# Performance work log

Measured on AMD Instinct MI355X. Metric: run time of the kernel, lower is better.

Reference implementation:

```python
import jax, jax.numpy as jnp
import numpy as np

N = 8192
IN_F = 512
OUT_F = 256
POW = 2


def setup_inputs() -> dict:
    key = jax.random.key(0)
    k1, k2, k3, k4 = jax.random.split(key, 4)
    stdv = 1.0 / np.sqrt(OUT_F)
    inputs = {
        "input": jax.random.normal(k1, (N, IN_F), dtype=jnp.float32),
        "adj": jax.random.uniform(k2, (N, N), dtype=jnp.float32),
        "weight": jax.random.uniform(k3, (IN_F, OUT_F), dtype=jnp.float32, minval=-stdv, maxval=stdv),
        "bias": jax.random.uniform(k4, (OUT_F,), dtype=jnp.float32, minval=-stdv, maxval=stdv),
    }
    return inputs


def reference(input, adj, weight, bias):
    # K_adj = adj ** pow (elementwise power, as torch's ** on a dense tensor)
    k_adj = adj ** POW
    # support = X @ W  -> [N, out_features]
    support = jnp.einsum("ni,io->no", input, weight)
    # output = K_adj @ support -> [N, out_features]
    out = jnp.einsum("nm,mo->no", k_adj, support) + bias
    # F.elu with default alpha=1.0
    return jnp.where(out > 0, out, jnp.expm1(out))
```

## Files before the change

### kernel.cpp

```cpp
#include <hip/hip_runtime.h>
#include <cstdint>
#include <cstddef>

#define N_NODES 8192
#define INF 512
#define OUTF 256
#define SPLITK 8
#define MSLICE (N_NODES / SPLITK)

typedef _Float16 f16;
typedef _Float16 f16x8 __attribute__((ext_vector_type(8)));
typedef float f32x4 __attribute__((ext_vector_type(4)));

__device__ __forceinline__ void async_copy16(void* lds_dst, const void* g_src) {
  __builtin_amdgcn_global_load_lds(
      (const __attribute__((address_space(1))) void*)g_src,
      (__attribute__((address_space(3))) void*)lds_dst,
      16, 0, 0);
}

__device__ __forceinline__ float elu(float x) { return x > 0.f ? x : expm1f(x); }

__global__ __launch_bounds__(256) void cast_x(const float* __restrict__ X,
                                              f16* __restrict__ Xh) {
  const int idx = blockIdx.x * 256 + threadIdx.x;
  f32x4 v0 = ((const f32x4*)X)[idx * 2];
  f32x4 v1 = ((const f32x4*)X)[idx * 2 + 1];
  f16x8 h;
#pragma unroll
  for (int u = 0; u < 4; ++u) {
    h[u] = (f16)v0[u];
    h[4 + u] = (f16)v1[u];
  }
  ((f16x8*)Xh)[idx] = h;
}

__global__ __launch_bounds__(256) void transpose_w(const float* __restrict__ W,
                                                   f16* __restrict__ WhT) {
  const int idx = blockIdx.x * 256 + threadIdx.x;
  const int o = idx >> 9, i = idx & 511;
  WhT[idx] = (f16)W[i * OUTF + o];
}

__global__ __launch_bounds__(256) void gemm1(const f16* __restrict__ WhT,
                                             const f16* __restrict__ Xh,
                                             f16* __restrict__ supT) {
  __shared__ __align__(16) f16 Asm[64 * 64];
  __shared__ __align__(16) f16 Bsm[128 * 64];
  const int t = threadIdx.x;
  const int wave = t >> 6, lane = t & 63;
  const int q = lane >> 4, r = lane & 15;
  const int lrow = lane >> 3, lchunk = lane & 7;
  const int o0 = blockIdx.x * 64, m0 = blockIdx.y * 128;

  f32x4 acc[4][2];
#pragma unroll
  for (int i = 0; i < 4; ++i)
#pragma unroll
    for (int j = 0; j < 2; ++j) acc[i][j] = (f32x4){0.f, 0.f, 0.f, 0.f};

  for (int kt = 0; kt < 8; ++kt) {
    const int k0 = kt * 64;
#pragma unroll
    for (int op = 0; op < 2; ++op) {
      const int row = (wave * 2 + op) * 8 + lrow;
      const f16* src = WhT + (size_t)(o0 + row) * INF + k0 + (lchunk ^ lrow) * 8;
      async_copy16(Asm + (wave * 2 + op) * 8 * 64, src);
    }
#pragma unroll
    for (int op = 0; op < 4; ++op) {
      const int row = (wave * 4 + op) * 8 + lrow;
      const f16* src = Xh + (size_t)(m0 + row) * INF + k0 + (lchunk ^ lrow) * 8;
      async_copy16(Bsm + (wave * 4 + op) * 8 * 64, src);
    }
    __syncthreads();
#pragma unroll
    for (int s = 0; s < 2; ++s) {
      const int pc = ((s * 4 + q) ^ (r & 7)) * 8;
      f16x8 af[4], bf[2];
#pragma unroll
      for (int i = 0; i < 4; ++i) af[i] = *(const f16x8*)&Asm[(i * 16 + r) * 64 + pc];
#pragma unroll
      for (int j = 0; j < 2; ++j)
        bf[j] = *(const f16x8*)&Bsm[(wave * 32 + j * 16 + r) * 64 + pc];
#pragma unroll
      for (int i = 0; i < 4; ++i)
#pragma unroll
        for (int j = 0; j < 2; ++j)
          acc[i][j] = __builtin_amdgcn_mfma_f32_16x16x32_f16(af[i], bf[j],
                                                             acc[i][j], 0, 0, 0);
    }
    __syncthreads();
  }
#pragma unroll
  for (int i = 0; i < 4; ++i)
#pragma unroll
    for (int j = 0; j < 2; ++j) {
      const int m = m0 + wave * 32 + j * 16 + r;
#pragma unroll
      for (int g = 0; g < 4; ++g)
        supT[(size_t)(o0 + i * 16 + q * 4 + g) * N_NODES + m] = (f16)acc[i][j][g];
    }
}

template <bool ATOMIC>
__global__ __launch_bounds__(256, 4) void gemm2(const float* __restrict__ adj,
                                                const f16* __restrict__ supT,
                                                float* __restrict__ outp) {
  __shared__ __align__(16) f16 Asm[64 * 64];
  __shared__ __align__(16) f16 Bsm[256 * 64];
  const int t = threadIdx.x;
  const int wave = t >> 6, lane = t & 63;
  const int q = lane >> 4, r = lane & 15;
  const int n0 = blockIdx.x * 64;
  const size_t m_base = (size_t)blockIdx.y * MSLICE;

  f32x4 acc[4][4];
#pragma unroll
  for (int i = 0; i < 4; ++i)
#pragma unroll
    for (int j = 0; j < 4; ++j) acc[i][j] = (f32x4){0.f, 0.f, 0.f, 0.f};

  const int a_row = t >> 2;
  const int a_c0 = (t & 3) * 2;
  const float* aptr = adj + (size_t)(n0 + a_row) * N_NODES + m_base + (t & 3) * 16;
  const int b_o = wave * 64 + (lane >> 3);
  const int b_kb = lane & 7;

  for (int kt = 0; kt < MSLICE / 64; ++kt) {
#pragma unroll
    for (int j = 0; j < 8; ++j) {
      const int o = b_o + j * 8;
      const int kb = b_kb ^ (o & 7);
      const f16* src = supT + (size_t)o * N_NODES + m_base + kt * 64 + kb * 8;
      async_copy16(Bsm + (wave * 64 + j * 8) * 64, src);
    }
    {
      const float* ap = aptr + kt * 64;
      f32x4 v0 = *(const f32x4*)(ap + 0);
      f32x4 v1 = *(const f32x4*)(ap + 4);
      f32x4 v2 = *(const f32x4*)(ap + 8);
      f32x4 v3 = *(const f32x4*)(ap + 12);
      f16x8 h0, h1;
#pragma unroll
      for (int u = 0; u < 4; ++u) {
        h0[u] = (f16)(v0[u] * v0[u]);
        h0[4 + u] = (f16)(v1[u] * v1[u]);
        h1[u] = (f16)(v2[u] * v2[u]);
        h1[4 + u] = (f16)(v3[u] * v3[u]);
      }
      *(f16x8*)&Asm[a_row * 64 + ((a_c0 ^ (a_row & 7)) * 8)] = h0;
      *(f16x8*)&Asm[a_row * 64 + (((a_c0 + 1) ^ (a_row & 7)) * 8)] = h1;
    }
    __syncthreads();
#pragma unroll
    for (int s = 0; s < 2; ++s) {
      const int pc = ((s * 4 + q) ^ (r & 7)) * 8;
      f16x8 af[4], bf[4];
#pragma unroll
      for (int i = 0; i < 4; ++i) af[i] = *(const f16x8*)&Asm[(i * 16 + r) * 64 + pc];
#pragma unroll
      for (int j = 0; j < 4; ++j)
        bf[j] = *(const f16x8*)&Bsm[(wave * 64 + j * 16 + r) * 64 + pc];
#pragma unroll
      for (int i = 0; i < 4; ++i)
#pragma unroll
        for (int j = 0; j < 4; ++j)
          acc[i][j] = __builtin_amdgcn_mfma_f32_16x16x32_f16(af[i], bf[j],
                                                             acc[i][j], 0, 0, 0);
    }
    __syncthreads();
  }
  float* base = ATOMIC ? outp : outp + (size_t)blockIdx.y * N_NODES * OUTF;
#pragma unroll
  for (int i = 0; i < 4; ++i)
#pragma unroll
    for (int g = 0; g < 4; ++g) {
      const int n = n0 + i * 16 + q * 4 + g;
      float* orow = base + (size_t)n * OUTF + wave * 64 + r;
#pragma unroll
      for (int j = 0; j < 4; ++j) {
        if (ATOMIC)
          atomicAdd(orow + j * 16, acc[i][j][g]);
        else
          orow[j * 16] = acc[i][j][g];
      }
    }
}

__global__ __launch_bounds__(256) void reduce_elu(const float* __restrict__ P,
                                                  const float* __restrict__ bias,
                                                  float* __restrict__ out) {
  const int idx = blockIdx.x * 256 + threadIdx.x;
  f32x4 s = (f32x4){0.f, 0.f, 0.f, 0.f};
#pragma unroll
  for (int y = 0; y < SPLITK; ++y)
    s += ((const f32x4*)(P + (size_t)y * N_NODES * OUTF))[idx];
  const f32x4 b = ((const f32x4*)bias)[idx & 63];
  f32x4 v;
#pragma unroll
  for (int u = 0; u < 4; ++u) v[u] = elu(s[u] + b[u]);
  ((f32x4*)out)[idx] = v;
}

__global__ __launch_bounds__(256) void bias_elu(float* __restrict__ out,
                                                const float* __restrict__ bias) {
  const int idx = blockIdx.x * 256 + threadIdx.x;
  f32x4 v = ((const f32x4*)out)[idx];
  const f32x4 b = ((const f32x4*)bias)[idx & 63];
#pragma unroll
  for (int u = 0; u < 4; ++u) v[u] = elu(v[u] + b[u]);
  ((f32x4*)out)[idx] = v;
}

extern "C" void kernel_launch(void* const* d_in, const int* in_sizes, int n_in,
                              void* d_out, int out_size, void* d_ws, size_t ws_size,
                              hipStream_t stream) {
  const float* X = (const float*)d_in[0];
  const float* adj = (const float*)d_in[1];
  const float* W = (const float*)d_in[2];
  const float* bias = (const float*)d_in[3];
  float* out = (float*)d_out;

  char* ws = (char*)d_ws;
  f16* supT = (f16*)(ws + 0);
  f16* Xh = (f16*)(ws + (4u << 20));
  f16* WhT = (f16*)(ws + (12u << 20));
  float* P = (float*)(ws + (16u << 20));
  const size_t need = (80u << 20);

  cast_x<<<N_NODES * INF / 8 / 256, 256, 0, stream>>>(X, Xh);
  transpose_w<<<INF * OUTF / 256, 256, 0, stream>>>(W, WhT);
  gemm1<<<dim3(OUTF / 64, N_NODES / 128), 256, 0, stream>>>(WhT, Xh, supT);
  if (ws_size >= need) {
    gemm2<false><<<dim3(N_NODES / 64, SPLITK), 256, 0, stream>>>(adj, supT, P);
    reduce_elu<<<N_NODES * OUTF / 4 / 256, 256, 0, stream>>>(P, bias, out);
  } else {
    hipMemsetAsync(d_out, 0, (size_t)out_size * sizeof(float), stream);
    gemm2<true><<<dim3(N_NODES / 64, SPLITK), 256, 0, stream>>>(adj, supT, out);
    bias_elu<<<N_NODES * OUTF / 4 / 256, 256, 0, stream>>>(out, bias);
  }
}
```

Measured before the change: 443.4 us.

## Fuse X cast into gemm1 and store split-K partials in f16

Removes the separate cast_x kernel by loading fp32 X directly in gemm1 and converting it to f16 while staging into LDS, with gemm1 tiles reduced to 64x64. Split-K partial sums from gemm2 are now written as f16 and reduced in fp32, which halves partial-buffer traffic and shrinks the workspace requirement. The cost is lower precision in the partial sums and a smaller gemm1 tile with less data reuse.

```diff
diff --git a/kernel.cpp b/kernel.cpp
--- a/kernel.cpp
+++ b/kernel.cpp
@@ -10,6 +10,7 @@
 
 typedef _Float16 f16;
 typedef _Float16 f16x8 __attribute__((ext_vector_type(8)));
+typedef _Float16 f16x4 __attribute__((ext_vector_type(4)));
 typedef float f32x4 __attribute__((ext_vector_type(4)));
 
 __device__ __forceinline__ void async_copy16(void* lds_dst, const void* g_src) {
@@ -21,43 +22,31 @@
 
 __device__ __forceinline__ float elu(float x) { return x > 0.f ? x : expm1f(x); }
 
-__global__ __launch_bounds__(256) void cast_x(const float* __restrict__ X,
-                                              f16* __restrict__ Xh) {
-  const int idx = blockIdx.x * 256 + threadIdx.x;
-  f32x4 v0 = ((const f32x4*)X)[idx * 2];
-  f32x4 v1 = ((const f32x4*)X)[idx * 2 + 1];
-  f16x8 h;
-#pragma unroll
-  for (int u = 0; u < 4; ++u) {
-    h[u] = (f16)v0[u];
-    h[4 + u] = (f16)v1[u];
-  }
-  ((f16x8*)Xh)[idx] = h;
-}
-
-__global__ __launch_bounds__(256) void transpose_w(const float* __restrict__ W,
-                                                   f16* __restrict__ WhT) {
+__global__ __launch_bounds__(256) void prep_w(const float* __restrict__ W,
+                                              f16* __restrict__ WhT) {
   const int idx = blockIdx.x * 256 + threadIdx.x;
   const int o = idx >> 9, i = idx & 511;
   WhT[idx] = (f16)W[i * OUTF + o];
 }
 
 __global__ __launch_bounds__(256) void gemm1(const f16* __restrict__ WhT,
-                                             const f16* __restrict__ Xh,
+                                             const float* __restrict__ X,
                                              f16* __restrict__ supT) {
   __shared__ __align__(16) f16 Asm[64 * 64];
-  __shared__ __align__(16) f16 Bsm[128 * 64];
+  __shared__ __align__(16) f16 Bsm[64 * 64];
   const int t = threadIdx.x;
   const int wave = t >> 6, lane = t & 63;
   const int q = lane >> 4, r = lane & 15;
   const int lrow = lane >> 3, lchunk = lane & 7;
-  const int o0 = blockIdx.x * 64, m0 = blockIdx.y * 128;
-
-  f32x4 acc[4][2];
-#pragma unroll
-  for (int i = 0; i < 4; ++i)
-#pragma unroll
-    for (int j = 0; j < 2; ++j) acc[i][j] = (f32x4){0.f, 0.f, 0.f, 0.f};
+  const int o0 = blockIdx.x * 64, m0 = blockIdx.y * 64;
+
+  f32x4 acc[4];
+#pragma unroll
+  for (int i = 0; i < 4; ++i) acc[i] = (f32x4){0.f, 0.f, 0.f, 0.f};
+
+  const int b_row = t >> 2;
+  const int b_c0 = (t & 3) * 2;
+  const float* xptr = X + (size_t)(m0 + b_row) * INF + (t & 3) * 16;
 
   for (int kt = 0; kt < 8; ++kt) {
     const int k0 = kt * 64;
@@ -65,47 +54,51 @@
     for (int op = 0; op < 2; ++op) {
       const int row = (wave * 2 + op) * 8 + lrow;
       const f16* src = WhT + (size_t)(o0 + row) * INF + k0 + (lchunk ^ lrow) * 8;
-      async_copy16(Asm + (wave * 2 + op) * 8 * 64, src);
-    }
-#pragma unroll
-    for (int op = 0; op < 4; ++op) {
-      const int row = (wave * 4 + op) * 8 + lrow;
-      const f16* src = Xh + (size_t)(m0 + row) * INF + k0 + (lchunk ^ lrow) * 8;
-      async_copy16(Bsm + (wave * 4 + op) * 8 * 64, src);
+      async_copy16(Asm + (wave * 2 + op) * 512, src);
+    }
+    {
+      const float* xp = xptr + k0;
+      f32x4 v0 = *(const f32x4*)(xp + 0);
+      f32x4 v1 = *(const f32x4*)(xp + 4);
+      f32x4 v2 = *(const f32x4*)(xp + 8);
+      f32x4 v3 = *(const f32x4*)(xp + 12);
+      f16x8 h0, h1;
+#pragma unroll
+      for (int u = 0; u < 4; ++u) {
+        h0[u] = (f16)v0[u];
+        h0[4 + u] = (f16)v1[u];
+        h1[u] = (f16)v2[u];
+        h1[4 + u] = (f16)v3[u];
+      }
+      *(f16x8*)&Bsm[b_row * 64 + ((b_c0 ^ (b_row & 7)) * 8)] = h0;
+      *(f16x8*)&Bsm[b_row * 64 + (((b_c0 + 1) ^ (b_row & 7)) * 8)] = h1;
     }
     __syncthreads();
 #pragma unroll
     for (int s = 0; s < 2; ++s) {
       const int pc = ((s * 4 + q) ^ (r & 7)) * 8;
-      f16x8 af[4], bf[2];
+      f16x8 af[4];
 #pragma unroll
       for (int i = 0; i < 4; ++i) af[i] = *(const f16x8*)&Asm[(i * 16 + r) * 64 + pc];
-#pragma unroll
-      for (int j = 0; j < 2; ++j)
-        bf[j] = *(const f16x8*)&Bsm[(wave * 32 + j * 16 + r) * 64 + pc];
+      const f16x8 bf = *(const f16x8*)&Bsm[(wave * 16 + r) * 64 + pc];
 #pragma unroll
       for (int i = 0; i < 4; ++i)
-#pragma unroll
-        for (int j = 0; j < 2; ++j)
-          acc[i][j] = __builtin_amdgcn_mfma_f32_16x16x32_f16(af[i], bf[j],
-                                                             acc[i][j], 0, 0, 0);
-    }
-    __syncthreads();
-  }
+        acc[i] = __builtin_amdgcn_mfma_f32_16x16x32_f16(af[i], bf, acc[i], 0, 0, 0);
+    }
+    __syncthreads();
+  }
+  const int m = m0 + wave * 16 + r;
 #pragma unroll
   for (int i = 0; i < 4; ++i)
 #pragma unroll
-    for (int j = 0; j < 2; ++j) {
-      const int m = m0 + wave * 32 + j * 16 + r;
-#pragma unroll
-      for (int g = 0; g < 4; ++g)
-        supT[(size_t)(o0 + i * 16 + q * 4 + g) * N_NODES + m] = (f16)acc[i][j][g];
-    }
+    for (int g = 0; g < 4; ++g)
+      supT[(size_t)(o0 + i * 16 + q * 4 + g) * N_NODES + m] = (f16)acc[i][g];
 }
 
 template <bool ATOMIC>
 __global__ __launch_bounds__(256, 4) void gemm2(const float* __restrict__ adj,
                                                 const f16* __restrict__ supT,
+                                                f16* __restrict__ P16,
                                                 float* __restrict__ outp) {
   __shared__ __align__(16) f16 Asm[64 * 64];
   __shared__ __align__(16) f16 Bsm[256 * 64];
@@ -171,31 +164,41 @@
     }
     __syncthreads();
   }
-  float* base = ATOMIC ? outp : outp + (size_t)blockIdx.y * N_NODES * OUTF;
-#pragma unroll
-  for (int i = 0; i < 4; ++i)
-#pragma unroll
-    for (int g = 0; g < 4; ++g) {
-      const int n = n0 + i * 16 + q * 4 + g;
-      float* orow = base + (size_t)n * OUTF + wave * 64 + r;
-#pragma unroll
-      for (int j = 0; j < 4; ++j) {
-        if (ATOMIC)
-          atomicAdd(orow + j * 16, acc[i][j][g]);
-        else
-          orow[j * 16] = acc[i][j][g];
-      }
-    }
-}
-
-__global__ __launch_bounds__(256) void reduce_elu(const float* __restrict__ P,
+  if (ATOMIC) {
+#pragma unroll
+    for (int i = 0; i < 4; ++i)
+#pragma unroll
+      for (int g = 0; g < 4; ++g) {
+        const int n = n0 + i * 16 + q * 4 + g;
+        float* orow = outp + (size_t)n * OUTF + wave * 64 + r;
+#pragma unroll
+        for (int j = 0; j < 4; ++j) atomicAdd(orow + j * 16, acc[i][j][g]);
+      }
+  } else {
+    f16* base = P16 + (size_t)blockIdx.y * N_NODES * OUTF;
+#pragma unroll
+    for (int i = 0; i < 4; ++i)
+#pragma unroll
+      for (int g = 0; g < 4; ++g) {
+        const int n = n0 + i * 16 + q * 4 + g;
+        f16* orow = base + (size_t)n * OUTF + wave * 64 + r;
+#pragma unroll
+        for (int j = 0; j < 4; ++j) orow[j * 16] = (f16)acc[i][j][g];
+      }
+  }
+}
+
+__global__ __launch_bounds__(256) void reduce_elu(const f16* __restrict__ P16,
                                                   const float* __restrict__ bias,
                                                   float* __restrict__ out) {
   const int idx = blockIdx.x * 256 + threadIdx.x;
   f32x4 s = (f32x4){0.f, 0.f, 0.f, 0.f};
 #pragma unroll
-  for (int y = 0; y < SPLITK; ++y)
-    s += ((const f32x4*)(P + (size_t)y * N_NODES * OUTF))[idx];
+  for (int y = 0; y < SPLITK; ++y) {
+    const f16x4 h = ((const f16x4*)(P16 + (size_t)y * N_NODES * OUTF))[idx];
+#pragma unroll
+    for (int u = 0; u < 4; ++u) s[u] += (float)h[u];
+  }
   const f32x4 b = ((const f32x4*)bias)[idx & 63];
   f32x4 v;
 #pragma unroll
@@ -224,20 +227,18 @@
 
   char* ws = (char*)d_ws;
   f16* supT = (f16*)(ws + 0);
-  f16* Xh = (f16*)(ws + (4u << 20));
-  f16* WhT = (f16*)(ws + (12u << 20));
-  float* P = (float*)(ws + (16u << 20));
-  const size_t need = (80u << 20);
-
-  cast_x<<<N_NODES * INF / 8 / 256, 256, 0, stream>>>(X, Xh);
-  transpose_w<<<INF * OUTF / 256, 256, 0, stream>>>(W, WhT);
-  gemm1<<<dim3(OUTF / 64, N_NODES / 128), 256, 0, stream>>>(WhT, Xh, supT);
+  f16* WhT = (f16*)(ws + (4u << 20));
+  f16* P16 = (f16*)(ws + (8u << 20));
+  const size_t need = (40u << 20);
+
+  prep_w<<<INF * OUTF / 256, 256, 0, stream>>>(W, WhT);
+  gemm1<<<dim3(OUTF / 64, N_NODES / 64), 256, 0, stream>>>(WhT, X, supT);
   if (ws_size >= need) {
-    gemm2<false><<<dim3(N_NODES / 64, SPLITK), 256, 0, stream>>>(adj, supT, P);
-    reduce_elu<<<N_NODES * OUTF / 4 / 256, 256, 0, stream>>>(P, bias, out);
+    gemm2<false><<<dim3(N_NODES / 64, SPLITK), 256, 0, stream>>>(adj, supT, P16, nullptr);
+    reduce_elu<<<N_NODES * OUTF / 4 / 256, 256, 0, stream>>>(P16, bias, out);
   } else {
     hipMemsetAsync(d_out, 0, (size_t)out_size * sizeof(float), stream);
-    gemm2<true><<<dim3(N_NODES / 64, SPLITK), 256, 0, stream>>>(adj, supT, out);
+    gemm2<true><<<dim3(N_NODES / 64, SPLITK), 256, 0, stream>>>(adj, supT, nullptr, out);
     bias_elu<<<N_NODES * OUTF / 4 / 256, 256, 0, stream>>>(out, bias);
   }
 }
```

Result: faster. 434.6 us (-2.0%).
